# Optimization experiments

Hardware: AMD Instinct MI355X
Metric: run time of the kernel (lower is better)

## Reference

```python
import jax, jax.numpy as jnp
import numpy as np


def setup_inputs() -> dict:
    key = jax.random.key(0)
    B, T, D = 16, 2048, 256
    inputs = jax.random.normal(key, (B, T, D), dtype=jnp.float32)
    return {"inputs": inputs, "window_size": 7}


def reference(inputs, window_size):
    # Faithful to the keras layer: output[b, t] = concat(x[t], x[t-1], ..., x[t-W+1])
    # with zeros where t-k < 0. Built with one pad + W shifted views instead of
    # the original O(W^2) pad/concat loop.
    B, T, D = inputs.shape
    W = window_size
    padded = jnp.pad(inputs, ((0, 0), (W - 1, 0), (0, 0)))  # [B, T+W-1, D]
    # slice k gives x shifted right by k (i.e., x[t-k]) over the valid range
    pieces = [padded[:, W - 1 - k : W - 1 - k + T, :] for k in range(W)]
    return jnp.concatenate(pieces, axis=2)  # [B, T, W*D]
```

## Files before the change

kernel.cpp:

```cpp
#include <hip/hip_runtime.h>


typedef float vf4 __attribute__((ext_vector_type(4)));

constexpr int B    = 16;
constexpr int T    = 2048;
constexpr int D    = 256;
constexpr int W    = 7;
constexpr int D4   = D / 4;
constexpr int ROW4 = W * D4;
constexpr int RPB  = 16;
constexpr int NROW = B * T;
constexpr int NBLK = NROW / RPB;

__global__ __launch_bounds__(W * 64) void window_gather_kernel(
    const vf4* __restrict__ in, vf4* __restrict__ out) {
  const int w  = threadIdx.x >> 6;
  const int dd = threadIdx.x & 63;
  const int r0 = blockIdx.x * RPB;
  const int t0 = r0 & (T - 1);

  vf4* dst = out + (size_t)r0 * ROW4 + w * D4 + dd;

  if (t0 != 0) {
    const vf4* src = in + (r0 - w) * D4 + dd;
    vf4 v[RPB];
#pragma unroll
    for (int i = 0; i < RPB; ++i) v[i] = src[i * D4];
#pragma unroll
    for (int i = 0; i < RPB; ++i) dst[i * ROW4] = v[i];
  } else {
    vf4 v[RPB];
#pragma unroll
    for (int i = 0; i < RPB; ++i) {
      int sr = r0 + i - w;
      if (sr < 0) sr = 0;
      vf4 ld = in[sr * D4 + dd];
      vf4 z  = {0.f, 0.f, 0.f, 0.f};
      v[i] = (i >= w) ? ld : z;
    }
#pragma unroll
    for (int i = 0; i < RPB; ++i) dst[i * ROW4] = v[i];
  }
}

extern "C" void kernel_launch(void* const* d_in, const int* in_sizes, int n_in,
                              void* d_out, int out_size, void* d_ws, size_t ws_size,
                              hipStream_t stream) {
  const vf4* in = (const vf4*)d_in[0];
  vf4* out = (vf4*)d_out;
  window_gather_kernel<<<NBLK, W * 64, 0, stream>>>(in, out);
}
```

Before: 259.8 us.

## Assign each wave a group of rows and reuse loaded inputs across window slots

Restructures the gather so each wavefront owns eight output rows, loads the needed span of input rows once into registers, and writes all window slots for each row contiguously. This replaces the earlier scheme where each of seven waves reloaded shifted input rows. The goal is to cut redundant input reads and make output writes sequential per row. It uses more registers per thread and gives each wave more work.

```diff
diff --git a/kernel.cpp b/kernel.cpp
--- a/kernel.cpp
+++ b/kernel.cpp
@@ -9,38 +9,40 @@
 constexpr int W    = 7;
 constexpr int D4   = D / 4;
 constexpr int ROW4 = W * D4;
-constexpr int RPB  = 16;
+constexpr int G    = 8;
+constexpr int NLD  = G + W - 1;
 constexpr int NROW = B * T;
-constexpr int NBLK = NROW / RPB;
+constexpr int NWAVE = NROW / G;
+constexpr int NBLK  = NWAVE / 4;
 
-__global__ __launch_bounds__(W * 64) void window_gather_kernel(
+__global__ __launch_bounds__(256) void window_waverow_kernel(
     const vf4* __restrict__ in, vf4* __restrict__ out) {
-  const int w  = threadIdx.x >> 6;
-  const int dd = threadIdx.x & 63;
-  const int r0 = blockIdx.x * RPB;
-  const int t0 = r0 & (T - 1);
+  const int wid  = (blockIdx.x << 2) | (threadIdx.x >> 6);
+  const int lane = threadIdx.x & 63;
+  const int r0   = wid * G;
+  const int t0   = r0 & (T - 1);
 
-  vf4* dst = out + (size_t)r0 * ROW4 + w * D4 + dd;
+  vf4 v[NLD];
+  if (t0 != 0) {
+    const vf4* src = in + (r0 - (W - 1)) * D4 + lane;
+#pragma unroll
+    for (int j = 0; j < NLD; ++j) v[j] = src[j * D4];
+  } else {
+    const vf4 z = {0.f, 0.f, 0.f, 0.f};
+#pragma unroll
+    for (int j = 0; j < W - 1; ++j) v[j] = z;
+    const vf4* src = in + r0 * D4 + lane;
+#pragma unroll
+    for (int j = 0; j < G; ++j) v[W - 1 + j] = src[j * D4];
+  }
 
-  if (t0 != 0) {
-    const vf4* src = in + (r0 - w) * D4 + dd;
-    vf4 v[RPB];
+  vf4* dst = out + (size_t)r0 * ROW4 + lane;
 #pragma unroll
-    for (int i = 0; i < RPB; ++i) v[i] = src[i * D4];
+  for (int i = 0; i < G; ++i) {
 #pragma unroll
-    for (int i = 0; i < RPB; ++i) dst[i * ROW4] = v[i];
-  } else {
-    vf4 v[RPB];
-#pragma unroll
-    for (int i = 0; i < RPB; ++i) {
-      int sr = r0 + i - w;
-      if (sr < 0) sr = 0;
-      vf4 ld = in[sr * D4 + dd];
-      vf4 z  = {0.f, 0.f, 0.f, 0.f};
-      v[i] = (i >= w) ? ld : z;
+    for (int w = 0; w < W; ++w) {
+      dst[i * ROW4 + w * D4] = v[i + (W - 1) - w];
     }
-#pragma unroll
-    for (int i = 0; i < RPB; ++i) dst[i * ROW4] = v[i];
   }
 }
 
@@ -49,5 +51,5 @@
                               hipStream_t stream) {
   const vf4* in = (const vf4*)d_in[0];
   vf4* out = (vf4*)d_out;
-  window_gather_kernel<<<NBLK, W * 64, 0, stream>>>(in, out);
+  window_waverow_kernel<<<NBLK, 256, 0, stream>>>(in, out);
 }
```

After: 263.7 us. About the same (+1.5%).
